# Optimization experiments

Hardware: AMD Instinct MI355X
Metric: run time of the kernel (lower is better)

The kernel has to match this reference:

```python
import jax, jax.numpy as jnp
import numpy as np

BLOCK = 128      # ModelArgs.block_size
FP8_MAX = 448.0  # e4m3 max, used by act_quant


def setup_inputs() -> dict:
    key = jax.random.key(0)
    k1, k2, k3 = jax.random.split(key, 3)
    M, K, O = 8192, 4096, 4096
    x = jax.random.normal(k1, (M, K), dtype=jnp.float32)
    # 'fp8' weight values (simulated in fp32) and blockwise fp32 scales
    weight = jax.random.normal(k2, (O, K), dtype=jnp.float32)
    w_scale = jax.random.uniform(k3, (O // BLOCK, K // BLOCK), dtype=jnp.float32,
                                 minval=0.5, maxval=1.5)
    return {"x": x, "weight": weight, "w_scale": w_scale}


def reference(x, weight, w_scale):
    M, K = x.shape
    O = weight.shape[0]
    Kb, Ob = K // BLOCK, O // BLOCK

    # --- act_quant: per-(row, k-block) scale = amax/448, quantized vals x/scale ---
    xb = x.reshape(M, Kb, BLOCK)
    sx = jnp.max(jnp.abs(xb), axis=-1, keepdims=True) / FP8_MAX  # [M, Kb, 1]
    xq = xb / sx                                                  # simulated fp8 activations

    # --- weight_dequant: blockwise scale expansion ---
    wdq = (weight.reshape(Ob, BLOCK, Kb, BLOCK) * w_scale[:, None, :, None]).reshape(O, K)

    # --- fp8_gemm: y = (xq * sx) @ wdq^T  (activation scales folded back per block) ---
    xd = (xq * sx).reshape(M, K)
    y = jnp.einsum('mk,ok->mo', xd, wdq)  # [M, O]
    return y
```

## Files before the change

kernel.cpp:

```cpp
#include <hip/hip_runtime.h>
#include <hip/hip_bf16.h>

#define M_DIM 8192
#define K_DIM 4096
#define O_DIM 4096
#define QB    128
#define BK    64

typedef __attribute__((ext_vector_type(8))) short  short8;
typedef __attribute__((ext_vector_type(4))) float  floatx4;

__device__ __forceinline__ short f2bf(float f) {
    unsigned u = __float_as_uint(f);
    unsigned r = u + 0x7fffu + ((u >> 16) & 1u);
    return (short)(r >> 16);
}

__global__ __launch_bounds__(512) void cvt_fused(const float* __restrict__ x,
                                                 const float* __restrict__ w,
                                                 const float* __restrict__ s,
                                                 short* __restrict__ xb,
                                                 short* __restrict__ wb) {
    const size_t NX = (size_t)M_DIM * K_DIM / 8;
    size_t t = (size_t)blockIdx.x * 512 + threadIdx.x;
    if (t < NX) {
        size_t i = t * 8;
        floatx4 f0 = __builtin_nontemporal_load((const floatx4*)(x + i));
        floatx4 f1 = __builtin_nontemporal_load((const floatx4*)(x + i + 4));
        short8 o;
        o[0] = f2bf(f0[0]); o[1] = f2bf(f0[1]); o[2] = f2bf(f0[2]); o[3] = f2bf(f0[3]);
        o[4] = f2bf(f1[0]); o[5] = f2bf(f1[1]); o[6] = f2bf(f1[2]); o[7] = f2bf(f1[3]);
        *(short8*)(xb + i) = o;
    } else {
        size_t i = (t - NX) * 8;
        int o = (int)(i >> 12);
        int k = (int)(i & (K_DIM - 1));
        float sc = s[(o >> 7) * (K_DIM / QB) + (k >> 7)];
        floatx4 f0 = __builtin_nontemporal_load((const floatx4*)(w + i));
        floatx4 f1 = __builtin_nontemporal_load((const floatx4*)(w + i + 4));
        short8 v;
        v[0] = f2bf(f0[0] * sc); v[1] = f2bf(f0[1] * sc);
        v[2] = f2bf(f0[2] * sc); v[3] = f2bf(f0[3] * sc);
        v[4] = f2bf(f1[0] * sc); v[5] = f2bf(f1[1] * sc);
        v[6] = f2bf(f1[2] * sc); v[7] = f2bf(f1[3] * sc);
        *(short8*)(wb + i) = v;
    }
}

__global__ __launch_bounds__(256) void gemm_bt(const short* __restrict__ A,
                                               const short* __restrict__ B,
                                               float* __restrict__ C) {
    __shared__ __align__(16) short lsA[128 * BK];
    __shared__ __align__(16) short lsB[128 * BK];

    const int tid  = threadIdx.x;
    const int lane = tid & 63;
    const int wave = tid >> 6;

    const int id  = blockIdx.x;
    const int xcd = id & 7;
    const int j   = id >> 3;
    const int bm  = j >> 2;
    const int bn  = (xcd << 2) | (j & 3);

    const int wm = (wave >> 1) << 6;
    const int wn = (wave & 1) << 6;

    const int sr = tid >> 3;
    const int sc = (((tid & 7) ^ (sr & 7)) << 3);
    const short* gA = A + (size_t)(bm * 128 + sr) * K_DIM + sc;
    const short* gB = B + (size_t)(bn * 128 + sr) * K_DIM + sc;

    floatx4 acc[4][4];
#pragma unroll
    for (int i = 0; i < 4; ++i)
#pragma unroll
        for (int jj = 0; jj < 4; ++jj)
            acc[i][jj] = (floatx4){0.f, 0.f, 0.f, 0.f};

    const int frow = lane & 15;
    const int fsw  = frow & 7;
    const int fc   = lane >> 4;

    for (int k0 = 0; k0 < K_DIM; k0 += BK) {
        __syncthreads();
#pragma unroll
        for (int g = 0; g < 4; ++g) {
            __builtin_amdgcn_global_load_lds(
                (const __attribute__((address_space(1))) void*)(gA + (size_t)(g * 32) * K_DIM),
                (__attribute__((address_space(3))) void*)&lsA[g * 2048 + tid * 8], 16, 0, 0);
            __builtin_amdgcn_global_load_lds(
                (const __attribute__((address_space(1))) void*)(gB + (size_t)(g * 32) * K_DIM),
                (__attribute__((address_space(3))) void*)&lsB[g * 2048 + tid * 8], 16, 0, 0);
        }
        gA += BK;
        gB += BK;
        __syncthreads();

#pragma unroll
        for (int ks = 0; ks < 2; ++ks) {
            const int pc = ((ks * 4 + fc) ^ fsw) << 3;
            short8 av[4], bv[4];
#pragma unroll
            for (int i = 0; i < 4; ++i)
                av[i] = *(const short8*)&lsA[(wm + i * 16 + frow) * BK + pc];
#pragma unroll
            for (int jj = 0; jj < 4; ++jj)
                bv[jj] = *(const short8*)&lsB[(wn + jj * 16 + frow) * BK + pc];
#pragma unroll
            for (int i = 0; i < 4; ++i)
#pragma unroll
                for (int jj = 0; jj < 4; ++jj)
                    acc[i][jj] = __builtin_amdgcn_mfma_f32_16x16x32_bf16(
                        av[i], bv[jj], acc[i][jj], 0, 0, 0);
        }
    }

    const int quad  = lane >> 4;
    const int crow0 = bm * 128 + wm + quad * 4;
    const int ccol0 = bn * 128 + wn + (lane & 15);
#pragma unroll
    for (int i = 0; i < 4; ++i)
#pragma unroll
        for (int jj = 0; jj < 4; ++jj) {
            float* cp = C + (size_t)(crow0 + i * 16) * O_DIM + (ccol0 + jj * 16);
#pragma unroll
            for (int r = 0; r < 4; ++r)
                cp[(size_t)r * O_DIM] = acc[i][jj][r];
        }
}

extern "C" void kernel_launch(void* const* d_in, const int* in_sizes, int n_in,
                              void* d_out, int out_size, void* d_ws, size_t ws_size,
                              hipStream_t stream) {
    const float* x  = (const float*)d_in[0];
    const float* w  = (const float*)d_in[1];
    const float* ws = (const float*)d_in[2];
    float* out = (float*)d_out;

    short* xb = (short*)d_ws;
    short* wb = xb + (size_t)M_DIM * K_DIM;

    const size_t total_t = ((size_t)M_DIM * K_DIM + (size_t)O_DIM * K_DIM) / 8;
    cvt_fused<<<(unsigned)(total_t / 512), 512, 0, stream>>>(x, w, ws, xb, wb);

    gemm_bt<<<(M_DIM / 128) * (O_DIM / 128), 256, 0, stream>>>(xb, wb, out);
}
```

Measured before the change: 489.1 us.

## Rewrite GEMM as 256x256 tile with double-buffered LDS and phased MFMA schedule

Replaces the 128x128, 4-wave single-buffer GEMM with a 256x256 tile run by 8 waves. Global-to-LDS loads are double-buffered, and the k-loop is split into barrier-separated MFMA phases with explicit waitcnt, sched_barrier and setprio, so loads overlap compute and tiles are reused more. It also drops the nontemporal loads in the conversion kernel. The risks are higher register pressure from 128 accumulator registers per lane, and fragile hand-written waitcnt and barrier logic.

```diff
diff --git a/kernel.cpp b/kernel.cpp
--- a/kernel.cpp
+++ b/kernel.cpp
@@ -1,14 +1,18 @@
 #include <hip/hip_runtime.h>
-#include <hip/hip_bf16.h>
 
 #define M_DIM 8192
 #define K_DIM 4096
 #define O_DIM 4096
 #define QB    128
 #define BK    64
+#define BMT   256
+#define BNT   256
 
 typedef __attribute__((ext_vector_type(8))) short  short8;
 typedef __attribute__((ext_vector_type(4))) float  floatx4;
+
+#define AS1 __attribute__((address_space(1)))
+#define AS3 __attribute__((address_space(3)))
 
 __device__ __forceinline__ short f2bf(float f) {
     unsigned u = __float_as_uint(f);
@@ -25,8 +29,8 @@
     size_t t = (size_t)blockIdx.x * 512 + threadIdx.x;
     if (t < NX) {
         size_t i = t * 8;
-        floatx4 f0 = __builtin_nontemporal_load((const floatx4*)(x + i));
-        floatx4 f1 = __builtin_nontemporal_load((const floatx4*)(x + i + 4));
+        floatx4 f0 = *(const floatx4*)(x + i);
+        floatx4 f1 = *(const floatx4*)(x + i + 4);
         short8 o;
         o[0] = f2bf(f0[0]); o[1] = f2bf(f0[1]); o[2] = f2bf(f0[2]); o[3] = f2bf(f0[3]);
         o[4] = f2bf(f1[0]); o[5] = f2bf(f1[1]); o[6] = f2bf(f1[2]); o[7] = f2bf(f1[3]);
@@ -36,8 +40,8 @@
         int o = (int)(i >> 12);
         int k = (int)(i & (K_DIM - 1));
         float sc = s[(o >> 7) * (K_DIM / QB) + (k >> 7)];
-        floatx4 f0 = __builtin_nontemporal_load((const floatx4*)(w + i));
-        floatx4 f1 = __builtin_nontemporal_load((const floatx4*)(w + i + 4));
+        floatx4 f0 = *(const floatx4*)(w + i);
+        floatx4 f1 = *(const floatx4*)(w + i + 4);
         short8 v;
         v[0] = f2bf(f0[0] * sc); v[1] = f2bf(f0[1] * sc);
         v[2] = f2bf(f0[2] * sc); v[3] = f2bf(f0[3] * sc);
@@ -47,86 +51,183 @@
     }
 }
 
-__global__ __launch_bounds__(256) void gemm_bt(const short* __restrict__ A,
-                                               const short* __restrict__ B,
-                                               float* __restrict__ C) {
-    __shared__ __align__(16) short lsA[128 * BK];
-    __shared__ __align__(16) short lsB[128 * BK];
+#define WAIT_LGKM asm volatile("s_waitcnt lgkmcnt(0)" ::: "memory")
+#define WAIT_VM4  asm volatile("s_waitcnt vmcnt(4)" ::: "memory")
+#define WAIT_VM0  asm volatile("s_waitcnt vmcnt(0)" ::: "memory")
+#define BARR      __builtin_amdgcn_s_barrier()
+#define SCHEDB    __builtin_amdgcn_sched_barrier(0)
+
+#define LDA4(DST, BUF, ROFF)                                                    \
+    _Pragma("unroll")                                                           \
+    for (int mi = 0; mi < 4; ++mi) {                                            \
+        DST[mi][0] = *(const short8*)&lsA[BUF][rA + (ROFF) + mi * 1024 + pc0];  \
+        DST[mi][1] = *(const short8*)&lsA[BUF][rA + (ROFF) + mi * 1024 + pc1];  \
+    }
+
+#define LDB2(DST, BUF, ROFF)                                                    \
+    _Pragma("unroll")                                                           \
+    for (int ni = 0; ni < 2; ++ni) {                                            \
+        DST[ni][0] = *(const short8*)&lsB[BUF][rB + (ROFF) + ni * 1024 + pc0];  \
+        DST[ni][1] = *(const short8*)&lsB[BUF][rB + (ROFF) + ni * 1024 + pc1];  \
+    }
+
+#define MM16(AF, BF, MO, NO)                                                    \
+    _Pragma("unroll")                                                           \
+    for (int mi = 0; mi < 4; ++mi)                                              \
+        _Pragma("unroll")                                                       \
+        for (int ni = 0; ni < 2; ++ni)                                          \
+            _Pragma("unroll")                                                   \
+            for (int ks = 0; ks < 2; ++ks)                                      \
+                acc[(MO) + mi][(NO) + ni] = __builtin_amdgcn_mfma_f32_16x16x32_bf16( \
+                    AF[mi][ks], BF[ni][ks], acc[(MO) + mi][(NO) + ni], 0, 0, 0);
+
+#define STAGE(LS, BUF, GP, KOFF, H)                                             \
+    __builtin_amdgcn_global_load_lds(                                           \
+        (const AS1 void*)((GP) + (size_t)((H) * 128) * K_DIM + (KOFF)),         \
+        (AS3 void*)&LS[BUF][(H) * 128 * BK + dst], 16, 0, 0);                   \
+    __builtin_amdgcn_global_load_lds(                                           \
+        (const AS1 void*)((GP) + (size_t)((H) * 128 + 64) * K_DIM + (KOFF)),    \
+        (AS3 void*)&LS[BUF][((H) * 128 + 64) * BK + dst], 16, 0, 0);
+
+#define MFMA_PH(...)                                                            \
+    BARR;                                                                       \
+    WAIT_LGKM;                                                                  \
+    SCHEDB;                                                                     \
+    __builtin_amdgcn_s_setprio(1);                                              \
+    __VA_ARGS__                                                                 \
+    __builtin_amdgcn_s_setprio(0);                                              \
+    BARR;                                                                       \
+    SCHEDB;
+
+__global__ __launch_bounds__(512, 2) void gemm_bt(const short* __restrict__ A,
+                                                  const short* __restrict__ B,
+                                                  float* __restrict__ C) {
+    __shared__ __align__(16) short lsA[2][BMT * BK];
+    __shared__ __align__(16) short lsB[2][BNT * BK];
 
     const int tid  = threadIdx.x;
     const int lane = tid & 63;
     const int wave = tid >> 6;
+    const int wr   = wave >> 2;
+    const int wc   = wave & 3;
 
     const int id  = blockIdx.x;
     const int xcd = id & 7;
     const int j   = id >> 3;
-    const int bm  = j >> 2;
-    const int bn  = (xcd << 2) | (j & 3);
-
-    const int wm = (wave >> 1) << 6;
-    const int wn = (wave & 1) << 6;
-
-    const int sr = tid >> 3;
-    const int sc = (((tid & 7) ^ (sr & 7)) << 3);
-    const short* gA = A + (size_t)(bm * 128 + sr) * K_DIM + sc;
-    const short* gB = B + (size_t)(bn * 128 + sr) * K_DIM + sc;
-
-    floatx4 acc[4][4];
-#pragma unroll
-    for (int i = 0; i < 4; ++i)
-#pragma unroll
-        for (int jj = 0; jj < 4; ++jj)
-            acc[i][jj] = (floatx4){0.f, 0.f, 0.f, 0.f};
+    const int bm  = j >> 1;
+    const int bn  = (xcd << 1) | (j & 1);
+
+    const int sr  = tid >> 3;
+    const int csw = ((tid & 7) ^ (sr & 7)) << 3;
+    const int dst = tid * 8;
+    const short* gA = A + (size_t)(bm * BMT + sr) * K_DIM + csw;
+    const short* gB = B + (size_t)(bn * BNT + sr) * K_DIM + csw;
 
     const int frow = lane & 15;
+    const int fc   = lane >> 4;
     const int fsw  = frow & 7;
-    const int fc   = lane >> 4;
-
-    for (int k0 = 0; k0 < K_DIM; k0 += BK) {
-        __syncthreads();
-#pragma unroll
-        for (int g = 0; g < 4; ++g) {
-            __builtin_amdgcn_global_load_lds(
-                (const __attribute__((address_space(1))) void*)(gA + (size_t)(g * 32) * K_DIM),
-                (__attribute__((address_space(3))) void*)&lsA[g * 2048 + tid * 8], 16, 0, 0);
-            __builtin_amdgcn_global_load_lds(
-                (const __attribute__((address_space(1))) void*)(gB + (size_t)(g * 32) * K_DIM),
-                (__attribute__((address_space(3))) void*)&lsB[g * 2048 + tid * 8], 16, 0, 0);
-        }
-        gA += BK;
-        gB += BK;
-        __syncthreads();
-
-#pragma unroll
-        for (int ks = 0; ks < 2; ++ks) {
-            const int pc = ((ks * 4 + fc) ^ fsw) << 3;
-            short8 av[4], bv[4];
-#pragma unroll
-            for (int i = 0; i < 4; ++i)
-                av[i] = *(const short8*)&lsA[(wm + i * 16 + frow) * BK + pc];
-#pragma unroll
-            for (int jj = 0; jj < 4; ++jj)
-                bv[jj] = *(const short8*)&lsB[(wn + jj * 16 + frow) * BK + pc];
-#pragma unroll
-            for (int i = 0; i < 4; ++i)
-#pragma unroll
-                for (int jj = 0; jj < 4; ++jj)
-                    acc[i][jj] = __builtin_amdgcn_mfma_f32_16x16x32_bf16(
-                        av[i], bv[jj], acc[i][jj], 0, 0, 0);
-        }
-    }
+    const int pc0  = (fc ^ fsw) << 3;
+    const int pc1  = ((4 + fc) ^ fsw) << 3;
+    const int rA   = (wr * 128 + frow) * BK;
+    const int rB   = (wc * 64 + frow) * BK;
+
+    floatx4 acc[8][4];
+#pragma unroll
+    for (int mi = 0; mi < 8; ++mi)
+#pragma unroll
+        for (int ni = 0; ni < 4; ++ni)
+            acc[mi][ni] = (floatx4){0.f, 0.f, 0.f, 0.f};
+
+    short8 a0[4][2], a1[4][2], b0[2][2], b1[2][2];
+
+    STAGE(lsA, 0, gA, 0, 0)
+    STAGE(lsA, 0, gA, 0, 1)
+    STAGE(lsB, 0, gB, 0, 0)
+    STAGE(lsB, 0, gB, 0, 1)
+    STAGE(lsA, 1, gA, 64, 0)
+    STAGE(lsA, 1, gA, 64, 1)
+    WAIT_VM4;
+    BARR;
+    SCHEDB;
+
+#pragma unroll 1
+    for (int it = 0; it < 31; ++it) {
+        LDA4(a0, 0, 0)
+        LDB2(b0, 0, 0)
+        STAGE(lsB, 1, gB, 64, 0)
+        MFMA_PH(MM16(a0, b0, 0, 0))
+
+        LDA4(a1, 0, 4096)
+        LDB2(b1, 0, 2048)
+        STAGE(lsB, 1, gB, 64, 1)
+        MFMA_PH(MM16(a0, b1, 0, 2))
+
+        STAGE(lsA, 0, gA, 128, 0)
+        MFMA_PH(MM16(a1, b0, 4, 0))
+
+        STAGE(lsA, 0, gA, 128, 1)
+        WAIT_VM4;
+        MFMA_PH(MM16(a1, b1, 4, 2))
+
+        LDA4(a0, 1, 0)
+        LDB2(b0, 1, 0)
+        STAGE(lsB, 0, gB, 128, 0)
+        MFMA_PH(MM16(a0, b0, 0, 0))
+
+        LDA4(a1, 1, 4096)
+        LDB2(b1, 1, 2048)
+        STAGE(lsB, 0, gB, 128, 1)
+        MFMA_PH(MM16(a0, b1, 0, 2))
+
+        STAGE(lsA, 1, gA, 192, 0)
+        MFMA_PH(MM16(a1, b0, 4, 0))
+
+        STAGE(lsA, 1, gA, 192, 1)
+        WAIT_VM4;
+        MFMA_PH(MM16(a1, b1, 4, 2))
+
+        gA += 2 * BK;
+        gB += 2 * BK;
+    }
+
+    LDA4(a0, 0, 0)
+    LDB2(b0, 0, 0)
+    STAGE(lsB, 1, gB, 64, 0)
+    MFMA_PH(MM16(a0, b0, 0, 0))
+
+    LDA4(a1, 0, 4096)
+    LDB2(b1, 0, 2048)
+    STAGE(lsB, 1, gB, 64, 1)
+    MFMA_PH(MM16(a0, b1, 0, 2))
+
+    MFMA_PH(MM16(a1, b0, 4, 0))
+
+    WAIT_VM0;
+    MFMA_PH(MM16(a1, b1, 4, 2))
+
+    LDA4(a0, 1, 0)
+    LDB2(b0, 1, 0)
+    MFMA_PH(MM16(a0, b0, 0, 0))
+
+    LDA4(a1, 1, 4096)
+    LDB2(b1, 1, 2048)
+    MFMA_PH(MM16(a0, b1, 0, 2))
+
+    MFMA_PH(MM16(a1, b0, 4, 0))
+
+    MFMA_PH(MM16(a1, b1, 4, 2))
 
     const int quad  = lane >> 4;
-    const int crow0 = bm * 128 + wm + quad * 4;
-    const int ccol0 = bn * 128 + wn + (lane & 15);
-#pragma unroll
-    for (int i = 0; i < 4; ++i)
-#pragma unroll
-        for (int jj = 0; jj < 4; ++jj) {
-            float* cp = C + (size_t)(crow0 + i * 16) * O_DIM + (ccol0 + jj * 16);
+    const int crow0 = bm * BMT + wr * 128 + quad * 4;
+    const int ccol0 = bn * BNT + wc * 64 + frow;
+#pragma unroll
+    for (int mi = 0; mi < 8; ++mi)
+#pragma unroll
+        for (int ni = 0; ni < 4; ++ni) {
+            float* cp = C + (size_t)(crow0 + mi * 16) * O_DIM + (ccol0 + ni * 16);
 #pragma unroll
             for (int r = 0; r < 4; ++r)
-                cp[(size_t)r * O_DIM] = acc[i][jj][r];
+                cp[(size_t)r * O_DIM] = acc[mi][ni][r];
         }
 }
 
@@ -144,5 +245,5 @@
     const size_t total_t = ((size_t)M_DIM * K_DIM + (size_t)O_DIM * K_DIM) / 8;
     cvt_fused<<<(unsigned)(total_t / 512), 512, 0, stream>>>(x, w, ws, xb, wb);
 
-    gemm_bt<<<(M_DIM / 128) * (O_DIM / 128), 256, 0, stream>>>(xb, wb, out);
-}
+    gemm_bt<<<(M_DIM / BMT) * (O_DIM / BNT), 512, 0, stream>>>(xb, wb, out);
+}
```

New measurement: 510.3 us. 1.04x slower.
